# Kernel optimization log

Measured on AMD Instinct MI355X. Metric: run time of the kernel, lower is better.

The kernel has to match this reference:

```python
import jax, jax.numpy as jnp
import numpy as np

N_NODES = 100000
N_EDGES = 3200000
IN_FEATS = 512
HIDDEN = 64
N_CLASSES = 32


def setup_inputs() -> dict:
    key = jax.random.key(0)
    k1, k2, k3, k4 = jax.random.split(key, 4)
    x = jax.random.normal(k1, (N_NODES, IN_FEATS), dtype=jnp.float32)
    edge_index = jax.random.randint(k2, (2, N_EDGES), 0, N_NODES, dtype=jnp.int64)
    # Glorot-ish init for weights
    W1 = jax.random.normal(k3, (IN_FEATS, HIDDEN), dtype=jnp.float32) / np.sqrt(IN_FEATS)
    b1 = jnp.zeros((HIDDEN,), dtype=jnp.float32)
    W2 = jax.random.normal(k4, (HIDDEN, N_CLASSES), dtype=jnp.float32) / np.sqrt(HIDDEN)
    b2 = jnp.zeros((N_CLASSES,), dtype=jnp.float32)
    return {"x": x, "edge_index": edge_index, "W1": W1, "b1": b1, "W2": W2, "b2": b2}


def reference(x, edge_index, W1, b1, W2, b2):
    N = x.shape[0]
    # GCNConv default: add self-loops, unit edge weights (edge_attr is None for Cora)
    loop = jnp.arange(N, dtype=edge_index.dtype)
    src = jnp.concatenate([edge_index[0], loop])  # [E+N]
    dst = jnp.concatenate([edge_index[1], loop])  # [E+N]
    w = jnp.ones(src.shape[0], dtype=x.dtype)
    # symmetric normalization: deg^-1/2[src] * w * deg^-1/2[dst]
    deg = jax.ops.segment_sum(w, dst, num_segments=N)
    dinv = jnp.where(deg > 0, jax.lax.rsqrt(deg), 0.0)
    norm = dinv[src] * w * dinv[dst]  # [E+N]

    def gcn_layer(h, W, b):
        h = h @ W                              # transform first (out dim small)
        msg = h[src] * norm[:, None]           # gather + scale  [E+N, d_out]
        agg = jax.ops.segment_sum(msg, dst, num_segments=N)  # scatter-add
        return agg + b

    h = jax.nn.relu(gcn_layer(x, W1, b1))
    # F.dropout(training=self.training) -> identity in eval mode
    out = gcn_layer(h, W2, b2)
    return jax.nn.log_softmax(out, axis=1)
```

## Files before the change

kernel.cpp:

```cpp
#include <hip/hip_runtime.h>
#include <hip/hip_fp16.h>
#include <math.h>

constexpr int N_NODES = 100000;
constexpr int N_EDGES = 3200000;
constexpr int IN_F = 512;
constexpr int HID = 64;
constexpr int NCLS = 32;
constexpr int CAP = 80;
constexpr int SHIFT = 9;
constexpr int NB = 196;
constexpr int BCAPC = 16976;
constexpr int CHUNK = 2048;
constexpr int SENT = N_NODES;

constexpr int GEMM1_BLOCKS = (N_NODES + 63) / 64;
constexpr int PART_BLOCKS  = (N_EDGES + CHUNK - 1) / CHUNK;

typedef short short8 __attribute__((ext_vector_type(8)));
typedef float f32x4 __attribute__((ext_vector_type(4)));
typedef int intx4 __attribute__((ext_vector_type(4)));

__device__ __forceinline__ unsigned short f2bf(float f) {
    union { float f; unsigned int u; } v; v.f = f;
    unsigned int r = (v.u + 0x7fffu + ((v.u >> 16) & 1u)) >> 16;
    return (unsigned short)r;
}
__device__ __forceinline__ float bf2f(unsigned short h) {
    union { unsigned int u; float f; } v; v.u = ((unsigned int)h) << 16;
    return v.f;
}
__device__ __forceinline__ unsigned char f2e5(float f) {
    unsigned short u = __half_as_ushort(__float2half(f));
    return (unsigned char)((u + 0x7Fu + ((u >> 8) & 1u)) >> 8);
}
__device__ __forceinline__ float e52f(unsigned char b) {
    return __half2float(__ushort_as_half((unsigned short)((unsigned short)b << 8)));
}

__global__ __launch_bounds__(256) void k_prep(const float* __restrict__ W1,
                                              unsigned short* __restrict__ W1T,
                                              unsigned char* __restrict__ h1s,
                                              unsigned char* __restrict__ h2s,
                                              int* __restrict__ gtail) {
    if (blockIdx.x == 128) {
        int t = threadIdx.x;
        if (t < HID)  h1s[(size_t)SENT * HID + t] = 0;
        if (t < NCLS) h2s[(size_t)SENT * NCLS + t] = 0;
        for (int i = t; i < NB * 16; i += 256) gtail[i] = 0;
        return;
    }
    int t = blockIdx.x * 256 + threadIdx.x;
    int k = t >> 6, c = t & 63;
    W1T[(size_t)c * IN_F + k] = f2bf(W1[(size_t)k * HID + c]);
}


__global__ __launch_bounds__(256) void k_part_gemm1(const int* __restrict__ src,
                                                    const int* __restrict__ dst,
                                                    int* __restrict__ gtail,
                                                    int* __restrict__ recs,
                                                    const float* __restrict__ x,
                                                    const unsigned short* __restrict__ W1T,
                                                    unsigned short* __restrict__ h1) {
    __shared__ alignas(16) char smem[13904];
    const int tid = threadIdx.x;
    const int wid = blockIdx.x >> 1;
    if (blockIdx.x & 1) {
        int* buf            = (int*)smem;
        unsigned char* bbuf = (unsigned char*)(smem + 8192);
        int* loc   = (int*)(smem + 10240);
        int* lh    = (int*)(smem + 11344);
        int* lbase = (int*)(smem + 12368);
        const int c0 = wid * CHUNK;
        const int cnum = min(CHUNK, N_EDGES - c0);
        lh[tid] = 0;
        __syncthreads();
        int dd[8], ss[8], rk[8];
        #pragma unroll
        for (int k = 0; k < 8; ++k) {
            int i = k * 256 + tid;
            if (i < cnum) {
                dd[k] = dst[c0 + i];
                ss[k] = src[c0 + i];
                rk[k] = atomicAdd(&lh[dd[k] >> SHIFT], 1);
            }
        }
        __syncthreads();
        int orig = lh[tid];
        loc[tid] = orig;
        __syncthreads();
        for (int off = 1; off < 256; off <<= 1) {
            int v = (tid >= off) ? loc[tid - off] : 0;
            __syncthreads();
            loc[tid] += v;
            __syncthreads();
        }
        int incl = loc[tid];
        __syncthreads();
        loc[tid] = incl - orig;
        if (tid == 255) loc[256] = incl;
        if (tid < NB && orig > 0) lbase[tid] = atomicAdd(&gtail[tid * 16], orig);
        __syncthreads();
        #pragma unroll
        for (int k = 0; k < 8; ++k) {
            int i = k * 256 + tid;
            if (i < cnum) {
                int b = dd[k] >> SHIFT;
                int pos = loc[b] + rk[k];
                buf[pos] = ((dd[k] & 511) << 17) | ss[k];
                bbuf[pos] = (unsigned char)b;
            }
        }
        __syncthreads();
        for (int i = tid; i < cnum; i += 256) {
            int b = bbuf[i];
            int idx = lbase[b] + (i - loc[b]);
            if (idx < BCAPC) recs[(size_t)b * BCAPC + idx] = buf[i];
        }
        return;
    }
    short* Xs = (short*)smem;
    short* Ws = (short*)(smem + 5120);
    const int row0 = wid * 64;
    const int w = tid >> 6;
    const int lane = tid & 63;
    const int r0l = (w >> 1) * 32;
    const int c0l = (w & 1) * 32;
    const int lrow = lane & 15;
    const int lkb = (lane >> 4) << 3;
    const int sr = tid >> 2;
    const int skq = (tid & 3) << 3;
    f32x4 acc00 = {0.f, 0.f, 0.f, 0.f}, acc01 = acc00, acc10 = acc00, acc11 = acc00;

    for (int k0 = 0; k0 < IN_F; k0 += 32) {
        {
            int grow = row0 + sr;
            short8 p = {0, 0, 0, 0, 0, 0, 0, 0};
            if (grow < N_NODES) {
                const float* xp = &x[(size_t)grow * IN_F + k0 + skq];
                float4 v0 = *reinterpret_cast<const float4*>(xp);
                float4 v1 = *reinterpret_cast<const float4*>(xp + 4);
                p[0] = (short)f2bf(v0.x); p[1] = (short)f2bf(v0.y);
                p[2] = (short)f2bf(v0.z); p[3] = (short)f2bf(v0.w);
                p[4] = (short)f2bf(v1.x); p[5] = (short)f2bf(v1.y);
                p[6] = (short)f2bf(v1.z); p[7] = (short)f2bf(v1.w);
            }
            *reinterpret_cast<short8*>(&Xs[sr * 40 + skq]) = p;
            *reinterpret_cast<short8*>(&Ws[sr * 40 + skq]) =
                *reinterpret_cast<const short8*>(&W1T[(size_t)sr * IN_F + k0 + skq]);
        }
        __syncthreads();
        short8 a0 = *reinterpret_cast<const short8*>(&Xs[(r0l + lrow) * 40 + lkb]);
        short8 a1 = *reinterpret_cast<const short8*>(&Xs[(r0l + 16 + lrow) * 40 + lkb]);
        short8 b0 = *reinterpret_cast<const short8*>(&Ws[(c0l + lrow) * 40 + lkb]);
        short8 b1 = *reinterpret_cast<const short8*>(&Ws[(c0l + 16 + lrow) * 40 + lkb]);
        acc00 = __builtin_amdgcn_mfma_f32_16x16x32_bf16(a0, b0, acc00, 0, 0, 0);
        acc01 = __builtin_amdgcn_mfma_f32_16x16x32_bf16(a0, b1, acc01, 0, 0, 0);
        acc10 = __builtin_amdgcn_mfma_f32_16x16x32_bf16(a1, b0, acc10, 0, 0, 0);
        acc11 = __builtin_amdgcn_mfma_f32_16x16x32_bf16(a1, b1, acc11, 0, 0, 0);
        __syncthreads();
    }
    const int vr0 = row0 + r0l + ((lane >> 4) << 2);
    const int gc0 = c0l + (lane & 15);
    #pragma unroll
    for (int v = 0; v < 4; ++v) {
        int gr = vr0 + v;
        if (gr < N_NODES) {
            h1[(size_t)gr * HID + gc0]      = f2bf(acc00[v]);
            h1[(size_t)gr * HID + gc0 + 16] = f2bf(acc01[v]);
        }
        int gr2 = gr + 16;
        if (gr2 < N_NODES) {
            h1[(size_t)gr2 * HID + gc0]      = f2bf(acc10[v]);
            h1[(size_t)gr2 * HID + gc0 + 16] = f2bf(acc11[v]);
        }
    }
}


__global__ __launch_bounds__(1024) void k_phase2(const int* __restrict__ gtail,
                                                 const int* __restrict__ recs,
                                                 int* __restrict__ slots,
                                                 int* __restrict__ cnt,
                                                 float* __restrict__ dinv,
                                                 const unsigned short* __restrict__ h1,
                                                 unsigned char* __restrict__ h1s) {
    __shared__ int scnt[512];
    const int b = blockIdx.x;
    const int tid = threadIdx.x;
    if (tid < 512) scnt[tid] = 0;
    __syncthreads();
    int nrec = min(gtail[b * 16], BCAPC);
    const int* rb = recs + (size_t)b * BCAPC;
    for (int i = tid; i < nrec; i += 1024) {
        int r = rb[i];
        int ln = r >> 17;
        int s  = r & 0x1FFFF;
        int p = atomicAdd(&scnt[ln], 1);
        int node = (b << SHIFT) + ln;
        if (p < CAP) slots[(size_t)node * CAP + p] = s;
    }
    __syncthreads();
    if (tid < 512) {
        int node = (b << SHIFT) + tid;
        if (node < N_NODES) {
            int c = scnt[tid];
            cnt[node] = c;
            dinv[node] = rsqrtf(1.0f + (float)c);
            int c2 = min(c, CAP);
            int degp = (c2 + 15) & ~15;
            for (int p = c2; p < degp; ++p) slots[(size_t)node * CAP + p] = SENT;
        }
    }
    for (int idx = tid; idx < 512 * 8; idx += 1024) {
        int ln = idx >> 3, g = idx & 7;
        int node = (b << SHIFT) + ln;
        if (node >= N_NODES) continue;
        float dv = rsqrtf(1.0f + (float)scnt[ln]);
        const unsigned short* hr = h1 + (size_t)node * HID;
        unsigned char* hs = h1s + (size_t)node * HID;
        short8 hv = *reinterpret_cast<const short8*>(hr + g * 8);
        unsigned int lo = 0, hi = 0;
        #pragma unroll
        for (int e = 0; e < 4; ++e)
            lo |= (unsigned int)f2e5(bf2f((unsigned short)hv[e]) * dv) << (e * 8);
        #pragma unroll
        for (int e = 0; e < 4; ++e)
            hi |= (unsigned int)f2e5(bf2f((unsigned short)hv[4 + e]) * dv) << (e * 8);
        *reinterpret_cast<uint2*>(hs + g * 8) = make_uint2(lo, hi);
    }
}


__global__ __launch_bounds__(256) void k_gather1(const int* __restrict__ cnt,
                                                 const int* __restrict__ slots,
                                                 const float* __restrict__ dinv,
                                                 const unsigned char* __restrict__ h1s,
                                                 const float* __restrict__ b1,
                                                 const float* __restrict__ W2,
                                                 unsigned char* __restrict__ h2s) {
    __shared__ alignas(16) float hsh[4][64];
    const int lane = threadIdx.x & 63;
    const int wv = threadIdx.x >> 6;
    const int cls = lane & 31;
    const int half = lane >> 5;
    float w[32];
    #pragma unroll
    for (int j = 0; j < 32; ++j)
        w[j] = W2[(size_t)(half * 32 + j) * NCLS + cls];
    const float bb = b1[lane];
    const int nw = gridDim.x * 4;
    for (int n0 = blockIdx.x * 4 + wv; n0 < N_NODES; n0 += nw) {
        const int n = __builtin_amdgcn_readfirstlane(n0);
        float dn = dinv[n];
        int deg = min(cnt[n], CAP);
        int degp = (deg + 15) & ~15;
        size_t base = (size_t)n * CAP;
        float a0 = e52f(h1s[(((unsigned)n) << 6) + lane]);
        float a1 = 0.f, a2 = 0.f, a3 = 0.f, a4 = 0.f, a5 = 0.f, a6 = 0.f, a7 = 0.f;
        for (int j = 0; j < degp; j += 16) {
            intx4 sa = __builtin_nontemporal_load(reinterpret_cast<const intx4*>(&slots[base + j]));
            intx4 sb = __builtin_nontemporal_load(reinterpret_cast<const intx4*>(&slots[base + j + 4]));
            intx4 sc = __builtin_nontemporal_load(reinterpret_cast<const intx4*>(&slots[base + j + 8]));
            intx4 sd = __builtin_nontemporal_load(reinterpret_cast<const intx4*>(&slots[base + j + 12]));
            a0 += e52f(h1s[(((unsigned)sa.x) << 6) + lane]);
            a1 += e52f(h1s[(((unsigned)sa.y) << 6) + lane]);
            a2 += e52f(h1s[(((unsigned)sa.z) << 6) + lane]);
            a3 += e52f(h1s[(((unsigned)sa.w) << 6) + lane]);
            a4 += e52f(h1s[(((unsigned)sb.x) << 6) + lane]);
            a5 += e52f(h1s[(((unsigned)sb.y) << 6) + lane]);
            a6 += e52f(h1s[(((unsigned)sb.z) << 6) + lane]);
            a7 += e52f(h1s[(((unsigned)sb.w) << 6) + lane]);
            a0 += e52f(h1s[(((unsigned)sc.x) << 6) + lane]);
            a1 += e52f(h1s[(((unsigned)sc.y) << 6) + lane]);
            a2 += e52f(h1s[(((unsigned)sc.z) << 6) + lane]);
            a3 += e52f(h1s[(((unsigned)sc.w) << 6) + lane]);
            a4 += e52f(h1s[(((unsigned)sd.x) << 6) + lane]);
            a5 += e52f(h1s[(((unsigned)sd.y) << 6) + lane]);
            a6 += e52f(h1s[(((unsigned)sd.z) << 6) + lane]);
            a7 += e52f(h1s[(((unsigned)sd.w) << 6) + lane]);
        }
        float v = fmaf(((a0 + a1) + (a2 + a3)) + ((a4 + a5) + (a6 + a7)), dn, bb);
        v = fmaxf(v, 0.f);
        hsh[wv][lane] = v;
        float acc = 0.f;
        #pragma unroll
        for (int q = 0; q < 8; ++q) {
            f32x4 hv = *reinterpret_cast<const f32x4*>(&hsh[wv][half * 32 + q * 4]);
            acc = fmaf(hv.x, w[q * 4 + 0], acc);
            acc = fmaf(hv.y, w[q * 4 + 1], acc);
            acc = fmaf(hv.z, w[q * 4 + 2], acc);
            acc = fmaf(hv.w, w[q * 4 + 3], acc);
        }
        acc += __shfl_xor(acc, 32, 64);
        if (half == 0)
            h2s[(((unsigned)n) << 5) + cls] = f2e5(acc * dn);
    }
}


__global__ __launch_bounds__(256) void k_out(const int* __restrict__ cnt,
                                             const int* __restrict__ slots,
                                             const float* __restrict__ dinv,
                                             const unsigned char* __restrict__ h2s,
                                             const float* __restrict__ b2,
                                             float* __restrict__ out) {
    int wid = blockIdx.x * 4 + (threadIdx.x >> 6);
    int n = __builtin_amdgcn_readfirstlane(wid);
    if (n >= N_NODES) return;
    int lane = threadIdx.x & 63;
    int cls = lane & 31;
    int half = lane >> 5;
    float dn = dinv[n];
    int deg = min(cnt[n], CAP);
    int degp = (deg + 15) & ~15;
    size_t base = (size_t)n * CAP;
    float a0 = half ? 0.f : e52f(h2s[(((unsigned)n) << 5) + cls]);
    float a1 = 0.f, a2 = 0.f, a3 = 0.f;
    for (int j = 0; j < degp; j += 16) {
        intx4 s0 = __builtin_nontemporal_load(
            reinterpret_cast<const intx4*>(&slots[base + j + half * 8]));
        intx4 s1 = __builtin_nontemporal_load(
            reinterpret_cast<const intx4*>(&slots[base + j + half * 8 + 4]));
        a0 += e52f(h2s[(((unsigned)s0.x) << 5) + cls]);
        a1 += e52f(h2s[(((unsigned)s0.y) << 5) + cls]);
        a2 += e52f(h2s[(((unsigned)s0.z) << 5) + cls]);
        a3 += e52f(h2s[(((unsigned)s0.w) << 5) + cls]);
        a0 += e52f(h2s[(((unsigned)s1.x) << 5) + cls]);
        a1 += e52f(h2s[(((unsigned)s1.y) << 5) + cls]);
        a2 += e52f(h2s[(((unsigned)s1.z) << 5) + cls]);
        a3 += e52f(h2s[(((unsigned)s1.w) << 5) + cls]);
    }
    float acc = (a0 + a1) + (a2 + a3);
    acc += __shfl_xor(acc, 32, 64);
    float z = fmaf(acc, dn, b2[cls]);
    float mx = z;
    #pragma unroll
    for (int d = 16; d > 0; d >>= 1) mx = fmaxf(mx, __shfl_xor(mx, d, 32));
    float ex = expf(z - mx);
    float sm = ex;
    #pragma unroll
    for (int d = 16; d > 0; d >>= 1) sm += __shfl_xor(sm, d, 32);
    if (half == 0)
        out[(size_t)n * NCLS + cls] = z - mx - logf(sm);
}


extern "C" void kernel_launch(void* const* d_in, const int* in_sizes, int n_in,
                              void* d_out, int out_size, void* d_ws, size_t ws_size,
                              hipStream_t stream) {
    const float* x  = (const float*)d_in[0];
    const int*   ei = (const int*)d_in[1];
    const float* W1 = (const float*)d_in[2];
    const float* b1 = (const float*)d_in[3];
    const float* W2 = (const float*)d_in[4];
    const float* b2 = (const float*)d_in[5];
    float* out = (float*)d_out;
    char* ws = (char*)d_ws;

    const int* src = ei;
    const int* dst = ei + N_EDGES;

    int*   gtail = (int*)ws;
    int*   cnt   = (int*)(ws + 16384);
    float* dinv  = (float*)(ws + 416384);
    unsigned short* W1T = (unsigned short*)(ws + 816384);
    int*   slots = (int*)(ws + 881920);
    unsigned short* h1 = (unsigned short*)(ws + 32882048ull);
    unsigned char* h1s = (unsigned char*)(ws + 45682048ull);
    char*  recs_base   = ws + 52082176ull;
    int*   recs  = (int*)recs_base;
    unsigned char* h2s  = (unsigned char*)(ws + 65391360ull);

    k_prep<<<129, 256, 0, stream>>>(W1, W1T, h1s, h2s, gtail);
    k_part_gemm1<<<GEMM1_BLOCKS + PART_BLOCKS, 256, 0, stream>>>(src, dst, gtail, recs, x, W1T, h1);
    k_phase2<<<NB, 1024, 0, stream>>>(gtail, recs, slots, cnt, dinv, h1, h1s);
    k_gather1<<<1536, 256, 0, stream>>>(cnt, slots, dinv, h1s, b1, W2, h2s);
    k_out<<<(N_NODES + 3) / 4, 256, 0, stream>>>(cnt, slots, dinv, h2s, b2, out);
}
```

Before: 208.4 us.

## Double-buffer GEMM1 tiles with register prefetch and use wave-shuffle scan in partition

The GEMM half of the fused kernel now prefetches the next x and W1T slices into registers while the current slice is multiplied. It alternates between two LDS buffers, which removes one barrier per k-step. The partition half replaces the 8-step LDS Hillis-Steele scan with a wavefront shuffle scan plus a cross-wave combine, which cuts the number of barriers. LDS use grows to about 20 KB per block, which may reduce occupancy.

```diff
diff --git a/kernel.cpp b/kernel.cpp
--- a/kernel.cpp
+++ b/kernel.cpp
@@ -63,15 +63,18 @@
                                                     const float* __restrict__ x,
                                                     const unsigned short* __restrict__ W1T,
                                                     unsigned short* __restrict__ h1) {
-    __shared__ alignas(16) char smem[13904];
+    __shared__ alignas(16) char smem[20608];
     const int tid = threadIdx.x;
     const int wid = blockIdx.x >> 1;
+    const int lane = tid & 63;
     if (blockIdx.x & 1) {
         int* buf            = (int*)smem;
         unsigned char* bbuf = (unsigned char*)(smem + 8192);
         int* loc   = (int*)(smem + 10240);
-        int* lh    = (int*)(smem + 11344);
-        int* lbase = (int*)(smem + 12368);
+        int* lh    = (int*)(smem + 11328);
+        int* lbase = (int*)(smem + 12352);
+        int* wsum  = (int*)(smem + 13376);
+        const int wv = tid >> 6;
         const int c0 = wid * CHUNK;
         const int cnum = min(CHUNK, N_EDGES - c0);
         lh[tid] = 0;
@@ -88,16 +91,18 @@
         }
         __syncthreads();
         int orig = lh[tid];
-        loc[tid] = orig;
-        __syncthreads();
-        for (int off = 1; off < 256; off <<= 1) {
-            int v = (tid >= off) ? loc[tid - off] : 0;
-            __syncthreads();
-            loc[tid] += v;
-            __syncthreads();
-        }
-        int incl = loc[tid];
-        __syncthreads();
+        int v = orig;
+        #pragma unroll
+        for (int off = 1; off < 64; off <<= 1) {
+            int t = __shfl_up(v, off, 64);
+            if (lane >= off) v += t;
+        }
+        if (lane == 63) wsum[wv] = v;
+        __syncthreads();
+        int pre = 0;
+        #pragma unroll
+        for (int k = 0; k < 4; ++k) if (k < wv) pre += wsum[k];
+        int incl = v + pre;
         loc[tid] = incl - orig;
         if (tid == 255) loc[256] = incl;
         if (tid < NB && orig > 0) lbase[tid] = atomicAdd(&gtail[tid * 16], orig);
@@ -120,11 +125,10 @@
         }
         return;
     }
-    short* Xs = (short*)smem;
-    short* Ws = (short*)(smem + 5120);
+    short* Xb = (short*)smem;
+    short* Wb = (short*)(smem + 10240);
     const int row0 = wid * 64;
     const int w = tid >> 6;
-    const int lane = tid & 63;
     const int r0l = (w >> 1) * 32;
     const int c0l = (w & 1) * 32;
     const int lrow = lane & 15;
@@ -133,33 +137,41 @@
     const int skq = (tid & 3) << 3;
     f32x4 acc00 = {0.f, 0.f, 0.f, 0.f}, acc01 = acc00, acc10 = acc00, acc11 = acc00;
 
-    for (int k0 = 0; k0 < IN_F; k0 += 32) {
-        {
-            int grow = row0 + sr;
-            short8 p = {0, 0, 0, 0, 0, 0, 0, 0};
-            if (grow < N_NODES) {
-                const float* xp = &x[(size_t)grow * IN_F + k0 + skq];
-                float4 v0 = *reinterpret_cast<const float4*>(xp);
-                float4 v1 = *reinterpret_cast<const float4*>(xp + 4);
-                p[0] = (short)f2bf(v0.x); p[1] = (short)f2bf(v0.y);
-                p[2] = (short)f2bf(v0.z); p[3] = (short)f2bf(v0.w);
-                p[4] = (short)f2bf(v1.x); p[5] = (short)f2bf(v1.y);
-                p[6] = (short)f2bf(v1.z); p[7] = (short)f2bf(v1.w);
-            }
-            *reinterpret_cast<short8*>(&Xs[sr * 40 + skq]) = p;
-            *reinterpret_cast<short8*>(&Ws[sr * 40 + skq]) =
-                *reinterpret_cast<const short8*>(&W1T[(size_t)sr * IN_F + k0 + skq]);
-        }
-        __syncthreads();
-        short8 a0 = *reinterpret_cast<const short8*>(&Xs[(r0l + lrow) * 40 + lkb]);
-        short8 a1 = *reinterpret_cast<const short8*>(&Xs[(r0l + 16 + lrow) * 40 + lkb]);
-        short8 b0 = *reinterpret_cast<const short8*>(&Ws[(c0l + lrow) * 40 + lkb]);
-        short8 b1 = *reinterpret_cast<const short8*>(&Ws[(c0l + 16 + lrow) * 40 + lkb]);
+    const int grow = row0 + sr;
+    const bool valid = grow < N_NODES;
+    const float* xp0 = &x[(size_t)grow * IN_F + skq];
+    const unsigned short* wp0 = &W1T[(size_t)sr * IN_F + skq];
+
+    float4 v0 = make_float4(0.f, 0.f, 0.f, 0.f), v1 = v0;
+    if (valid) { v0 = *reinterpret_cast<const float4*>(xp0);
+                 v1 = *reinterpret_cast<const float4*>(xp0 + 4); }
+    short8 wa = *reinterpret_cast<const short8*>(wp0);
+
+    #pragma unroll 4
+    for (int s = 0; s < 16; ++s) {
+        const int p = (s & 1) * 2560;
+        short8 px;
+        px[0] = (short)f2bf(v0.x); px[1] = (short)f2bf(v0.y);
+        px[2] = (short)f2bf(v0.z); px[3] = (short)f2bf(v0.w);
+        px[4] = (short)f2bf(v1.x); px[5] = (short)f2bf(v1.y);
+        px[6] = (short)f2bf(v1.z); px[7] = (short)f2bf(v1.w);
+        *reinterpret_cast<short8*>(&Xb[p + sr * 40 + skq]) = px;
+        *reinterpret_cast<short8*>(&Wb[p + sr * 40 + skq]) = wa;
+        __syncthreads();
+        if (s < 15) {
+            const float* xp = xp0 + (s + 1) * 32;
+            if (valid) { v0 = *reinterpret_cast<const float4*>(xp);
+                         v1 = *reinterpret_cast<const float4*>(xp + 4); }
+            wa = *reinterpret_cast<const short8*>(wp0 + (s + 1) * 32);
+        }
+        short8 a0 = *reinterpret_cast<const short8*>(&Xb[p + (r0l + lrow) * 40 + lkb]);
+        short8 a1 = *reinterpret_cast<const short8*>(&Xb[p + (r0l + 16 + lrow) * 40 + lkb]);
+        short8 b0 = *reinterpret_cast<const short8*>(&Wb[p + (c0l + lrow) * 40 + lkb]);
+        short8 b1 = *reinterpret_cast<const short8*>(&Wb[p + (c0l + 16 + lrow) * 40 + lkb]);
         acc00 = __builtin_amdgcn_mfma_f32_16x16x32_bf16(a0, b0, acc00, 0, 0, 0);
         acc01 = __builtin_amdgcn_mfma_f32_16x16x32_bf16(a0, b1, acc01, 0, 0, 0);
         acc10 = __builtin_amdgcn_mfma_f32_16x16x32_bf16(a1, b0, acc10, 0, 0, 0);
         acc11 = __builtin_amdgcn_mfma_f32_16x16x32_bf16(a1, b1, acc11, 0, 0, 0);
-        __syncthreads();
     }
     const int vr0 = row0 + r0l + ((lane >> 4) << 2);
     const int gc0 = c0l + (lane & 15);
```

After: 205.2 us. No clear change (-1.5%).
